# Kernel optimization log

Measured on AMD Instinct MI355X. Metric: run time of the kernel, lower is better.

Reference implementation:

```python
import jax, jax.numpy as jnp
import numpy as np

N_DISEASES = 8192
N_MIRNAS = 16384
N_TOTAL = N_DISEASES + N_MIRNAS
D = 256
B = 65536
K = 50
EPS = 1e-8


def setup_inputs() -> dict:
    key = jax.random.key(0)
    k1, k2, k3, k4, k5, k6 = jax.random.split(key, 6)
    h = jax.random.normal(k1, (N_TOTAL, D), dtype=jnp.float32)
    emb = jax.random.normal(k2, (N_TOTAL, D), dtype=jnp.float32)
    src_init = jax.random.normal(k3, (B, D), dtype=jnp.float32)
    dst_init = jax.random.normal(k4, (B, D), dtype=jnp.float32)
    diseases = jax.random.randint(k5, (B,), 0, N_DISEASES, dtype=jnp.int32)
    mirnas = jax.random.randint(k6, (B,), N_DISEASES, N_TOTAL, dtype=jnp.int32)
    return {"h": h, "emb": emb, "src_init": src_init, "dst_init": dst_init,
            "diseases": diseases, "mirnas": mirnas}


def _cos(a, b):
    # cosine similarity along the last axis, eps-clamped like torch's F.cosine_similarity
    na = jnp.maximum(jnp.linalg.norm(a, axis=-1), EPS)
    nb = jnp.maximum(jnp.linalg.norm(b, axis=-1), EPS)
    return jnp.sum(a * b, axis=-1) / (na * nb)


def _pair_contrastive(pos_sim, neg_sim):
    # -log(exp(pos) / (exp(pos) + exp(neg))) = logaddexp(0, neg - pos)
    return jnp.mean(jnp.logaddexp(jnp.float32(0.0), neg_sim - pos_sim))


def _knn_feature_update(features, k):
    # [N, N] dense similarity, top-(k+1), drop self, gather + mean
    sim = features @ features.T                      # [N, N]
    _, idx = jax.lax.top_k(sim, k + 1)               # [N, k+1]
    idx = idx[:, 1:]                                 # drop self-match
    nbr = features[idx]                              # [N, k, D]
    return jnp.mean(nbr, axis=1)                     # [N, D]


def _knn_contrastive(feat_a, feat_b):
    center_a = jnp.mean(feat_a, axis=0)
    center_b = jnp.mean(feat_b, axis=0)
    sa_a = _cos(feat_a, center_a[None, :])
    sb_a = _cos(feat_a, center_b[None, :])
    loss_a = _pair_contrastive(sa_a, sb_a)
    sb_b = _cos(feat_b, center_b[None, :])
    sa_b = _cos(feat_b, center_a[None, :])
    loss_b = _pair_contrastive(sb_b, sa_b)
    return (loss_a + loss_b) * jnp.float32(0.5)


def reference(h, emb, src_init, dst_init, diseases, mirnas):
    h_d = h[diseases]                                # [B, D]
    h_m = h[mirnas]                                  # [B, D]
    pos_sim = _cos(h_d, src_init)
    neg_sim = _cos(h_d, dst_init)
    contrastive_loss = _pair_contrastive(pos_sim, neg_sim)

    upd_d = _knn_feature_update(emb[:N_DISEASES], K)
    upd_m = _knn_feature_update(emb[N_DISEASES:], K)
    feature_contrastive_loss = _knn_contrastive(upd_d, upd_m)

    # interactionPredictor modeled as sigmoid dot-product scorer
    scores = jax.nn.sigmoid(jnp.sum(h_d * h_m, axis=-1))  # [B]
    return scores, contrastive_loss, feature_contrastive_loss
```

## Files before the change

kernel.cpp:

```cpp
#include <hip/hip_runtime.h>
#include <math.h>

#define NDIS 8192
#define NMIR 16384
#define NTOT 24576
#define DIMD 256
#define BPAIR 65536
#define KSEL 50
#define EPSF 1e-8f
#define CBC 32
#define CAP 80
#define PSTR 320
#define ZD 2.066f
#define ZM 2.418f
#define ZFD 0.9035f
#define ZFM 1.331f
#define NKB 768

typedef __attribute__((ext_vector_type(8))) short bf16x8;
typedef __attribute__((ext_vector_type(4))) float f32x4;
typedef unsigned long long ull;

__device__ __forceinline__ float wredsum(float v) {
#pragma unroll
  for (int off = 1; off < 64; off <<= 1) v += __shfl_xor(v, off, 64);
  return v;
}

__device__ __forceinline__ int wredsumi(int v) {
#pragma unroll
  for (int off = 1; off < 64; off <<= 1) v += __shfl_xor(v, off, 64);
  return v;
}

__device__ __forceinline__ float softplusf(float x) {
  return fmaxf(x, 0.0f) + log1pf(expf(-fabsf(x)));
}

__device__ __forceinline__ float dot4f(const float4 a, const float4 b) {
  return a.x * b.x + a.y * b.y + a.z * b.z + a.w * b.w;
}

__device__ __forceinline__ unsigned short f2bf(float f) {
  unsigned u = __float_as_uint(f);
  unsigned r = (u + 0x7fffu + ((u >> 16) & 1u)) >> 16;
  return (unsigned short)r;
}

__device__ __forceinline__ float b2f(unsigned short x) {
  return __uint_as_float((unsigned)x << 16);
}

__device__ __forceinline__ unsigned ordu(float f) {
  unsigned u = __float_as_uint(f);
  return (u & 0x80000000u) ? ~u : (u | 0x80000000u);
}

__global__ __launch_bounds__(256) void convert_colsum_kernel(
    const float* __restrict__ in, unsigned short* __restrict__ out,
    float* __restrict__ colpart) {
  const int d = threadIdx.x;
  const int r0 = blockIdx.x * 256;
  float s = 0.0f;
  for (int i = 0; i < 256; ++i) {
    const float v = in[(size_t)(r0 + i) * DIMD + d];
    const unsigned short b = f2bf(v);
    out[(size_t)(r0 + i) * DIMD + d] = b;
    s += b2f(b);
  }
  colpart[blockIdx.x * DIMD + d] = s;
}

__global__ __launch_bounds__(256) void tau_kernel(
    const unsigned short* __restrict__ embb, const float* __restrict__ colpart,
    float* __restrict__ tau, float2* __restrict__ musig,
    unsigned* __restrict__ cnts, unsigned* __restrict__ flags) {
  __shared__ float cm[DIMD];
  const int lane = threadIdx.x & 63;
  const int widx = threadIdx.x >> 6;
  const bool bism = blockIdx.x >= 32;
  {
    const int b0 = bism ? 32 : 0, b1 = bism ? 96 : 32;
    const float Ninv = 1.0f / (bism ? (float)NMIR : (float)NDIS);
    float s = 0.0f;
    for (int b = b0; b < b1; ++b) s += colpart[b * DIMD + threadIdx.x];
    cm[threadIdx.x] = s * Ninv;
  }
  __syncthreads();
  const int r0 = blockIdx.x * 256 + widx * 64;
  const float z = bism ? ZM : ZD;
  for (int rr = 0; rr < 64; ++rr) {
    const int row = r0 + rr;
    const float4 cmv = ((const float4*)cm)[lane];
    const ushort4 u = ((const ushort4*)(embb + (size_t)row * DIMD))[lane];
    const float fx = b2f(u.x), fy = b2f(u.y), fz = b2f(u.z), fw = b2f(u.w);
    float dot = fx * cmv.x + fy * cmv.y + fz * cmv.z + fw * cmv.w;
    float nsq = fx * fx + fy * fy + fz * fz + fw * fw;
    dot = wredsum(dot);
    nsq = wredsum(nsq);
    const float sig = sqrtf(nsq);
    if (lane == 0) {
      tau[row] = dot + z * sig;
      musig[row] = make_float2(dot, sig);
      flags[row] = 0u;
    }
    if (lane < 4) cnts[row * 4 + lane] = 0u;
  }
}

__global__ __launch_bounds__(256, 3) void knn_kernel(
    const unsigned short* __restrict__ embb, const float* __restrict__ tau,
    unsigned* __restrict__ part, unsigned* __restrict__ cnts,
    unsigned* __restrict__ flags, const float* __restrict__ h,
    const float* __restrict__ srci, const float* __restrict__ dsti,
    const int* __restrict__ dis, const int* __restrict__ mir,
    float* __restrict__ scores, float* __restrict__ pairpart) {
  __shared__ char lds[3][CBC * 512];
  __shared__ float wsum[4];

  const int tid = threadIdx.x;
  const int lane = tid & 63;
  const int widx = tid >> 6;
  const int q4 = lane >> 4;
  const int l15 = lane & 15;
  const int sh16 = q4 * 16;
  const unsigned lmask = (1u << l15) - 1u;

  const int bid = blockIdx.x;
  const bool ism = bid < 512;
  const int rt = ism ? (bid >> 2) : ((bid - 512) >> 2);
  const int strip = ism ? (bid & 3) : ((bid - 512) & 3);
  const int sw = ism ? 4096 : 2048;
  const int nch = sw / CBC;
  const int gbase = ism ? NDIS : 0;
  const unsigned short* fb = embb + (size_t)gbase * DIMD;

  const int rowbase = rt * 128 + widx * 32;
  const int colstart = strip * sw;
  const char* gb = (const char*)fb;

  bf16x8 afr[2][8];
#pragma unroll
  for (int rg = 0; rg < 2; ++rg) {
    const int arow = rowbase + rg * 16 + l15;
    const char* ab = (const char*)fb + (size_t)arow * 512 + q4 * 16;
#pragma unroll
    for (int kk = 0; kk < 8; ++kk)
      afr[rg][kk] = *(const bf16x8*)(ab + (size_t)kk * 64);
  }

  float tau8[2][4];
  unsigned offb[2];
  int cnt8[2][4];
#pragma unroll
  for (int rg = 0; rg < 2; ++rg) {
    const int db = rowbase + rg * 16 + q4 * 4;
    offb[rg] = (unsigned)(gbase + db) * PSTR + strip * CAP;
#pragma unroll
    for (int j = 0; j < 4; ++j) {
      tau8[rg][j] = tau[gbase + db + j];
      cnt8[rg][j] = 0;
    }
  }

  auto stage = [&](char* dst, int cb0n) {
#pragma unroll
    for (int it = 0; it < 4; ++it) {
      const int m = widx * 4 + it;
      const int col = m * 2 + (lane >> 5);
      const int qq = (lane & 31) * 16;
      const int koff = qq ^ ((col & 7) << 4);
      const char* src = gb + (size_t)(colstart + cb0n + col) * 512 + koff;
      __builtin_amdgcn_global_load_lds(
          (const __attribute__((address_space(1))) void*)src,
          (__attribute__((address_space(3))) void*)(dst + m * 1024), 16, 0, 0);
    }
  };

  char* b0 = lds[0];
  char* b1 = lds[1];
  char* b2 = lds[2];
  stage(b0, 0);
  stage(b1, CBC);
  for (int ch = 0; ch < nch; ++ch) {
    if (ch < nch - 1)
      asm volatile("s_waitcnt vmcnt(4)" ::: "memory");
    else
      asm volatile("s_waitcnt vmcnt(0)" ::: "memory");
    __builtin_amdgcn_sched_barrier(0);
    __builtin_amdgcn_s_barrier();
    __builtin_amdgcn_sched_barrier(0);
    if (ch + 2 < nch) stage(b2, (ch + 2) * CBC);

    const char* bch = b0;
    const int cb0 = ch * CBC;
    f32x4 acc[2][2];
#pragma unroll
    for (int rg = 0; rg < 2; ++rg)
#pragma unroll
      for (int t = 0; t < 2; ++t) acc[rg][t] = (f32x4){0.f, 0.f, 0.f, 0.f};

    __builtin_amdgcn_s_setprio(1);
#pragma unroll
    for (int t = 0; t < 2; ++t) {
      const int col = t * 16 + l15;
      const char* bbase = bch + (size_t)col * 512;
      const int xr = (col & 7) << 4;
#pragma unroll
      for (int kk = 0; kk < 8; ++kk) {
        const int koff = (kk * 64 + (q4 * 16)) ^ xr;
        const bf16x8 b = *(const bf16x8*)(bbase + koff);
        acc[0][t] = __builtin_amdgcn_mfma_f32_16x16x32_bf16(afr[0][kk], b,
                                                            acc[0][t], 0, 0, 0);
        acc[1][t] = __builtin_amdgcn_mfma_f32_16x16x32_bf16(afr[1][kk], b,
                                                            acc[1][t], 0, 0, 0);
      }
    }
    __builtin_amdgcn_s_setprio(0);

#pragma unroll
    for (int t = 0; t < 2; ++t) {
      const int colb = colstart + cb0 + t * 16;
      const unsigned kc = (unsigned)(16383 - (colb + l15));
#pragma unroll
      for (int rg = 0; rg < 2; ++rg) {
        const bool dchr = (colb == rowbase + rg * 16);
#pragma unroll
        for (int j = 0; j < 4; ++j) {
          const float v = acc[rg][t][j];
          bool ok = v > tau8[rg][j];
          if (dchr) ok = ok && (l15 != (q4 * 4 + j));
          const ull m = __ballot(ok);
          if (m) {
            const unsigned m16 = (unsigned)(m >> sh16) & 0xFFFFu;
            const int rank = __popc(m16 & lmask);
            const int slot = cnt8[rg][j] + rank;
            if (ok && slot < CAP)
              part[offb[rg] + (unsigned)(j * PSTR) + slot] =
                  ((ordu(v) >> 14) << 14) | kc;
            cnt8[rg][j] += __popc(m16);
          }
        }
      }
    }

    char* tp = b0; b0 = b1; b1 = b2; b2 = tp;
  }

#pragma unroll
  for (int rg = 0; rg < 2; ++rg) {
#pragma unroll
    for (int j = 0; j < 4; ++j) {
      if (l15 == 0) {
        const int growg = gbase + rowbase + rg * 16 + q4 * 4 + j;
        const int c = cnt8[rg][j];
        cnts[growg * 4 + strip] = (unsigned)(c < CAP ? c : CAP);
        if (c > CAP) flags[growg] = 1u;
      }
    }
  }

  const int gw = bid * 4 + widx;
  float lsum = 0.0f;
  for (int b = gw; b < BPAIR; b += NKB * 4) {
    const int d = dis[b];
    const int m = mir[b];
    const float4 a4 = ((const float4*)(h + (size_t)d * DIMD))[lane];
    const float4 m4 = ((const float4*)(h + (size_t)m * DIMD))[lane];
    const float4 s4 = ((const float4*)(srci + (size_t)b * DIMD))[lane];
    const float4 t4 = ((const float4*)(dsti + (size_t)b * DIMD))[lane];
    float aa = dot4f(a4, a4);
    float ss = dot4f(s4, s4);
    float tt = dot4f(t4, t4);
    float as = dot4f(a4, s4);
    float at = dot4f(a4, t4);
    float am = dot4f(a4, m4);
    aa = wredsum(aa); ss = wredsum(ss); tt = wredsum(tt);
    as = wredsum(as); at = wredsum(at); am = wredsum(am);
    const float ra = fmaxf(sqrtf(aa), EPSF);
    const float pos = as / (ra * fmaxf(sqrtf(ss), EPSF));
    const float neg = at / (ra * fmaxf(sqrtf(tt), EPSF));
    lsum += softplusf(neg - pos);
    if (lane == 0) scores[b] = 1.0f / (1.0f + expf(-am));
  }
  if (lane == 0) wsum[widx] = lsum;
  __syncthreads();
  if (tid == 0)
    pairpart[bid] = (wsum[0] + wsum[1]) + (wsum[2] + wsum[3]);
}

__global__ __launch_bounds__(256) void fallback_kernel(
    const unsigned short* __restrict__ embb, const float2* __restrict__ musig,
    unsigned* __restrict__ part, unsigned* __restrict__ cnts,
    const unsigned* __restrict__ flags, unsigned* __restrict__ fbbuf) {
  __shared__ unsigned short frow[4][DIMD];
  const int lane = threadIdx.x & 63;
  const int widx = threadIdx.x >> 6;
  const int wid = blockIdx.x * 4 + widx;
  const ull bel = (1ull << lane) - 1ull;

  for (int row = wid * 96; row < wid * 96 + 96; ++row) {
    unsigned tot = 0;
    for (int s = 0; s < 4; ++s) tot += cnts[row * 4 + s];
    if (!(flags[row] || tot < KSEL)) continue;

    const bool ism = row >= NDIS;
    const int lrow = ism ? row - NDIS : row;
    const int Ng = ism ? NMIR : NDIS;
    const unsigned short* fb = embb + (ism ? (size_t)NDIS * DIMD : 0);
    const float2 ms = musig[row];
    const float tp = ms.x + (ism ? ZFM : ZFD) * ms.y;

    ((ushort4*)frow[widx])[lane] =
        ((const ushort4*)(fb + (size_t)lrow * DIMD))[lane];

    unsigned* fk = fbbuf + (size_t)wid * 4096;
    int fc = 0;
    for (int cb = 0; cb < Ng; cb += 64) {
      const int col = cb + lane;
      float s = 0.0f;
      for (int d0 = 0; d0 < DIMD; d0 += 4) {
        const ushort4 uc = *(const ushort4*)(fb + (size_t)col * DIMD + d0);
        const ushort4 ur = *(const ushort4*)(&frow[widx][d0]);
        s += b2f(uc.x) * b2f(ur.x) + b2f(uc.y) * b2f(ur.y) +
             b2f(uc.z) * b2f(ur.z) + b2f(uc.w) * b2f(ur.w);
      }
      const bool a = (s > tp) && (col != lrow);
      const ull m = __ballot(a);
      const int sl = fc + __popcll(m & bel);
      if (a && sl < 4096) fk[sl] = ((ordu(s) >> 14) << 14) | (16383u - col);
      fc += __popcll(m);
    }
    if (fc > 4096) fc = 4096;

    unsigned lo = 0u, hi = 0xFFFFFFFFu;
    for (int it = 0; it < 32; ++it) {
      const unsigned mid = lo + ((hi - lo) >> 1);
      int c = 0;
      for (int i = lane; i < fc; i += 64) c += (fk[i] > mid) ? 1 : 0;
      c = wredsumi(c);
      if (c >= KSEL) lo = mid; else hi = mid;
    }
    int wc = 0;
    for (int base = 0; base < fc; base += 64) {
      const int i = base + lane;
      const bool w = (i < fc) && (fk[i] > lo);
      const ull m = __ballot(w);
      const int pos = wc + __popcll(m & bel);
      if (w) part[(size_t)row * PSTR + pos] = fk[i];
      wc += __popcll(m);
    }
    if (lane < 4) cnts[row * 4 + lane] = (lane == 0) ? KSEL : 0u;
  }
}

__global__ __launch_bounds__(256) void merge_kernel(
    const unsigned short* __restrict__ embb, const unsigned* __restrict__ part,
    const unsigned* __restrict__ cnts, float* __restrict__ upd_d,
    float* __restrict__ upd_m) {
  __shared__ unsigned kb[4][PSTR];
  const int lane = threadIdx.x & 63;
  const int widx = threadIdx.x >> 6;
  const int row = blockIdx.x * 4 + widx;
  const bool ism = row >= NDIS;
  const int lrow = ism ? row - NDIS : row;
  const unsigned short* fe = embb + (ism ? (size_t)NDIS * DIMD : 0);
  float* upd =
      (ism ? upd_m + (size_t)lrow * DIMD : upd_d + (size_t)lrow * DIMD);
  const ull bel = (1ull << lane) - 1ull;

  int T = 0;
  for (int s = 0; s < 4; ++s) {
    const int c = (int)cnts[row * 4 + s];
    for (int i = lane; i < c; i += 64)
      kb[widx][T + i] = part[(size_t)row * PSTR + s * CAP + i];
    T += c;
  }
  const int nr = (T + 63) >> 6;
  unsigned k[5];
#pragma unroll
  for (int i = 0; i < 5; ++i) {
    const int idx = i * 64 + lane;
    k[i] = (idx < T) ? kb[widx][idx] : 0u;
  }

  unsigned lo = 0u, hi = 0xFFFFFFFFu;
  for (int it = 0; it < 32; ++it) {
    const unsigned mid = lo + ((hi - lo) >> 1);
    int c = 0;
#pragma unroll
    for (int i = 0; i < 5; ++i)
      if (i < nr) c += __popcll(__ballot(k[i] > mid));
    if (c >= KSEL) lo = mid; else hi = mid;
  }
  int wc = 0;
#pragma unroll
  for (int i = 0; i < 5; ++i) {
    if (i < nr) {
      const bool w = k[i] > lo;
      const ull m = __ballot(w);
      const int pos = wc + __popcll(m & bel);
      if (w) kb[widx][pos] = 16383u - (k[i] & 16383u);
      wc += __popcll(m);
    }
  }

  float ax = 0.f, ay = 0.f, az = 0.f, aw = 0.f;
#pragma unroll 10
  for (int t = 0; t < KSEL; ++t) {
    const int col = (int)kb[widx][t];
    const ushort4 u = ((const ushort4*)(fe + (size_t)col * DIMD))[lane];
    ax += b2f(u.x); ay += b2f(u.y); az += b2f(u.z); aw += b2f(u.w);
  }
  const float inv = 1.0f / (float)KSEL;
  float4 o;
  o.x = ax * inv; o.y = ay * inv; o.z = az * inv; o.w = aw * inv;
  ((float4*)upd)[lane] = o;
}

__global__ __launch_bounds__(256) void center_partial(
    const float* __restrict__ upd, float* __restrict__ part) {
  const int c = threadIdx.x;
  const int r0 = blockIdx.x * 128;
  float s = 0.0f;
  for (int i = 0; i < 128; ++i) s += upd[(size_t)(r0 + i) * DIMD + c];
  part[blockIdx.x * DIMD + c] = s;
}

__global__ __launch_bounds__(256) void center_final(
    const float* __restrict__ part, float* __restrict__ center,
    float* __restrict__ cnorm) {
  const int g = blockIdx.x;
  const int c = threadIdx.x;
  const int b0 = g ? 64 : 0, b1 = g ? 192 : 64;
  const float N = g ? (float)NMIR : (float)NDIS;
  float s = 0.0f;
  for (int b = b0; b < b1; ++b) s += part[b * DIMD + c];
  s /= N;
  center[g * DIMD + c] = s;
  __shared__ float red[256];
  red[c] = s * s;
  __syncthreads();
  for (int off = 128; off > 0; off >>= 1) {
    if (c < off) red[c] += red[c + off];
    __syncthreads();
  }
  if (c == 0) cnorm[g] = sqrtf(red[0]);
}

__global__ __launch_bounds__(256) void knn_loss(
    const float* __restrict__ upd_d, const float* __restrict__ upd_m,
    const float* __restrict__ centers, const float* __restrict__ cnorms,
    float* __restrict__ lpa, float* __restrict__ lpb) {
  const int lane = threadIdx.x & 63;
  const int widx = threadIdx.x >> 6;
  const int bid = blockIdx.x;
  const bool ism = bid >= 128;
  const int lb = ism ? bid - 128 : bid;
  const int N = ism ? NMIR : NDIS;
  const int nw = ism ? 1024 : 512;
  const float* upd = ism ? upd_m : upd_d;
  const int gw = lb * 4 + widx;
  const float4 ca = ((const float4*)centers)[lane];
  const float4 cbv = ((const float4*)(centers + DIMD))[lane];
  const float na = fmaxf(cnorms[0], EPSF);
  const float nb = fmaxf(cnorms[1], EPSF);
  float lsum = 0.0f;
  for (int r = gw; r < N; r += nw) {
    const float4 u = ((const float4*)(upd + (size_t)r * DIMD))[lane];
    float uu = dot4f(u, u);
    float uca = dot4f(u, ca);
    float ucb = dot4f(u, cbv);
    uu = wredsum(uu); uca = wredsum(uca); ucb = wredsum(ucb);
    const float nu = fmaxf(sqrtf(uu), EPSF);
    const float sa = uca / (nu * na);
    const float sb = ucb / (nu * nb);
    const float x = ism ? (sa - sb) : (sb - sa);
    lsum += softplusf(x);
  }
  __shared__ float wsum[4];
  if (lane == 0) wsum[widx] = lsum;
  __syncthreads();
  if (threadIdx.x == 0) {
    const float v = (wsum[0] + wsum[1]) + (wsum[2] + wsum[3]);
    if (ism) lpb[lb] = v; else lpa[lb] = v;
  }
}

__global__ __launch_bounds__(256) void finalize_kernel(
    const float* __restrict__ pairpart, const float* __restrict__ lpa,
    const float* __restrict__ lpb, float* __restrict__ out) {
  __shared__ float red[256];
  const int t = threadIdx.x;

  float s = 0.0f;
  for (int i = t; i < NKB; i += 256) s += pairpart[i];
  red[t] = s;
  __syncthreads();
  for (int off = 128; off > 0; off >>= 1) {
    if (t < off) red[t] += red[t + off];
    __syncthreads();
  }
  const float pairsum = red[0];
  __syncthreads();

  red[t] = (t < 128) ? lpa[t] : 0.0f;
  __syncthreads();
  for (int off = 128; off > 0; off >>= 1) {
    if (t < off) red[t] += red[t + off];
    __syncthreads();
  }
  const float la = red[0];
  __syncthreads();

  red[t] = lpb[t];
  __syncthreads();
  for (int off = 128; off > 0; off >>= 1) {
    if (t < off) red[t] += red[t + off];
    __syncthreads();
  }
  const float lb = red[0];

  if (t == 0) {
    out[BPAIR] = pairsum / (float)BPAIR;
    out[BPAIR + 1] = 0.5f * (la / (float)NDIS + lb / (float)NMIR);
  }
}

extern "C" void kernel_launch(void* const* d_in, const int* in_sizes, int n_in,
                              void* d_out, int out_size, void* d_ws,
                              size_t ws_size, hipStream_t stream) {
  const float* h = (const float*)d_in[0];
  const float* emb = (const float*)d_in[1];
  const float* srci = (const float*)d_in[2];
  const float* dsti = (const float*)d_in[3];
  const int* dis = (const int*)d_in[4];
  const int* mir = (const int*)d_in[5];
  float* out = (float*)d_out;

  float* W = (float*)d_ws;
  float* upd_d = W;
  float* upd_m = upd_d + (size_t)NDIS * DIMD;
  float* pairpart = upd_m + (size_t)NMIR * DIMD;
  float* cpart = pairpart + 1024;
  float* centers = cpart + 192 * DIMD;
  float* cnorms = centers + 512;
  float* lpa = cnorms + 64;
  float* lpb = lpa + 128;
  float* colpart = lpb + 256;
  float* tau = colpart + 96 * DIMD;
  float2* musig = (float2*)(tau + NTOT);
  unsigned* flags = (unsigned*)(musig + NTOT);
  unsigned* cnts = flags + NTOT;
  unsigned short* embb = (unsigned short*)(cnts + NTOT * 4);
  unsigned* part = (unsigned*)(embb + (size_t)NTOT * DIMD);
  unsigned* fbbuf = part + (size_t)NTOT * PSTR;

  convert_colsum_kernel<<<96, 256, 0, stream>>>(emb, embb, colpart);
  tau_kernel<<<96, 256, 0, stream>>>(embb, colpart, tau, musig, cnts, flags);
  knn_kernel<<<NKB, 256, 0, stream>>>(embb, tau, part, cnts, flags, h, srci,
                                      dsti, dis, mir, out, pairpart);
  fallback_kernel<<<64, 256, 0, stream>>>(embb, musig, part, cnts, flags,
                                          fbbuf);
  merge_kernel<<<NTOT / 4, 256, 0, stream>>>(embb, part, cnts, upd_d, upd_m);
  center_partial<<<192, 256, 0, stream>>>(upd_d, cpart);
  center_final<<<2, 256, 0, stream>>>(cpart, centers, cnorms);
  knn_loss<<<384, 256, 0, stream>>>(upd_d, upd_m, centers, cnorms, lpa, lpb);
  finalize_kernel<<<1, 256, 0, stream>>>(pairpart, lpa, lpb, out);
}
```

Baseline: 513.7 us.

## Widen convert grid, add colmean kernel, precompute LDS read offsets in knn

The bf16 convert/column-sum kernel now runs 768 blocks of 32 rows instead of 96 blocks of 256 rows. A new two-block colmean kernel reduces the partial sums once, so tau_kernel no longer re-reduces them in every block. In the knn MFMA loop, the swizzled LDS read addresses are precomputed per lane as even/odd base offsets outside the chunk loop, buffers are addressed by integer offset, and the s_setprio bracketing is removed. The costs are one extra kernel launch and a larger colpart workspace; dropping setprio may change how waves interleave.

```diff
diff --git a/kernel.cpp b/kernel.cpp
--- a/kernel.cpp
+++ b/kernel.cpp
@@ -60,9 +60,9 @@
     const float* __restrict__ in, unsigned short* __restrict__ out,
     float* __restrict__ colpart) {
   const int d = threadIdx.x;
-  const int r0 = blockIdx.x * 256;
+  const int r0 = blockIdx.x * 32;
   float s = 0.0f;
-  for (int i = 0; i < 256; ++i) {
+  for (int i = 0; i < 32; ++i) {
     const float v = in[(size_t)(r0 + i) * DIMD + d];
     const unsigned short b = f2bf(v);
     out[(size_t)(r0 + i) * DIMD + d] = b;
@@ -71,21 +71,26 @@
   colpart[blockIdx.x * DIMD + d] = s;
 }
 
+__global__ __launch_bounds__(256) void colmean_kernel(
+    const float* __restrict__ colpart, float* __restrict__ colmean) {
+  const int g = blockIdx.x;
+  const int d = threadIdx.x;
+  const int b0 = g ? 256 : 0, b1 = g ? 768 : 256;
+  const float Ninv = 1.0f / (g ? (float)NMIR : (float)NDIS);
+  float s = 0.0f;
+  for (int b = b0; b < b1; ++b) s += colpart[b * DIMD + d];
+  colmean[g * DIMD + d] = s * Ninv;
+}
+
 __global__ __launch_bounds__(256) void tau_kernel(
-    const unsigned short* __restrict__ embb, const float* __restrict__ colpart,
+    const unsigned short* __restrict__ embb, const float* __restrict__ colmean,
     float* __restrict__ tau, float2* __restrict__ musig,
     unsigned* __restrict__ cnts, unsigned* __restrict__ flags) {
   __shared__ float cm[DIMD];
   const int lane = threadIdx.x & 63;
   const int widx = threadIdx.x >> 6;
   const bool bism = blockIdx.x >= 32;
-  {
-    const int b0 = bism ? 32 : 0, b1 = bism ? 96 : 32;
-    const float Ninv = 1.0f / (bism ? (float)NMIR : (float)NDIS);
-    float s = 0.0f;
-    for (int b = b0; b < b1; ++b) s += colpart[b * DIMD + threadIdx.x];
-    cm[threadIdx.x] = s * Ninv;
-  }
+  cm[threadIdx.x] = colmean[(bism ? DIMD : 0) + threadIdx.x];
   __syncthreads();
   const int r0 = blockIdx.x * 256 + widx * 64;
   const float z = bism ? ZM : ZD;
@@ -115,7 +120,7 @@
     const float* __restrict__ srci, const float* __restrict__ dsti,
     const int* __restrict__ dis, const int* __restrict__ mir,
     float* __restrict__ scores, float* __restrict__ pairpart) {
-  __shared__ char lds[3][CBC * 512];
+  __shared__ char lds[3 * CBC * 512];
   __shared__ float wsum[4];
 
   const int tid = threadIdx.x;
@@ -149,6 +154,16 @@
       afr[rg][kk] = *(const bf16x8*)(ab + (size_t)kk * 64);
   }
 
+  const int s6 = ((l15 >> 2) & 1) * 64;
+  const int Lc = (q4 * 16) ^ ((l15 & 3) << 4);
+  int vE[2], vO[2];
+#pragma unroll
+  for (int t = 0; t < 2; ++t) {
+    const int base = t * 8192 + l15 * 512 + Lc;
+    vE[t] = base + s6;
+    vO[t] = base - s6;
+  }
+
   float tau8[2][4];
   unsigned offb[2];
   int cnt8[2][4];
@@ -163,7 +178,7 @@
     }
   }
 
-  auto stage = [&](char* dst, int cb0n) {
+  auto stage = [&](int dstOff, int cb0n) {
 #pragma unroll
     for (int it = 0; it < 4; ++it) {
       const int m = widx * 4 + it;
@@ -173,15 +188,14 @@
       const char* src = gb + (size_t)(colstart + cb0n + col) * 512 + koff;
       __builtin_amdgcn_global_load_lds(
           (const __attribute__((address_space(1))) void*)src,
-          (__attribute__((address_space(3))) void*)(dst + m * 1024), 16, 0, 0);
+          (__attribute__((address_space(3))) void*)(lds + dstOff + m * 1024),
+          16, 0, 0);
     }
   };
 
-  char* b0 = lds[0];
-  char* b1 = lds[1];
-  char* b2 = lds[2];
-  stage(b0, 0);
-  stage(b1, CBC);
+  int o0 = 0, o1 = 16384, o2 = 32768;
+  stage(o0, 0);
+  stage(o1, CBC);
   for (int ch = 0; ch < nch; ++ch) {
     if (ch < nch - 1)
       asm volatile("s_waitcnt vmcnt(4)" ::: "memory");
@@ -190,9 +204,8 @@
     __builtin_amdgcn_sched_barrier(0);
     __builtin_amdgcn_s_barrier();
     __builtin_amdgcn_sched_barrier(0);
-    if (ch + 2 < nch) stage(b2, (ch + 2) * CBC);
-
-    const char* bch = b0;
+    if (ch + 2 < nch) stage(o2, (ch + 2) * CBC);
+
     const int cb0 = ch * CBC;
     f32x4 acc[2][2];
 #pragma unroll
@@ -200,23 +213,24 @@
 #pragma unroll
       for (int t = 0; t < 2; ++t) acc[rg][t] = (f32x4){0.f, 0.f, 0.f, 0.f};
 
-    __builtin_amdgcn_s_setprio(1);
 #pragma unroll
     for (int t = 0; t < 2; ++t) {
-      const int col = t * 16 + l15;
-      const char* bbase = bch + (size_t)col * 512;
-      const int xr = (col & 7) << 4;
-#pragma unroll
-      for (int kk = 0; kk < 8; ++kk) {
-        const int koff = (kk * 64 + (q4 * 16)) ^ xr;
-        const bf16x8 b = *(const bf16x8*)(bbase + koff);
-        acc[0][t] = __builtin_amdgcn_mfma_f32_16x16x32_bf16(afr[0][kk], b,
+      const char* pE = lds + o0 + vE[t];
+      const char* pO = lds + o0 + vO[t];
+#pragma unroll
+      for (int kp = 0; kp < 4; ++kp) {
+        const bf16x8 be = *(const bf16x8*)(pE + kp * 128);
+        acc[0][t] = __builtin_amdgcn_mfma_f32_16x16x32_bf16(afr[0][2 * kp], be,
                                                             acc[0][t], 0, 0, 0);
-        acc[1][t] = __builtin_amdgcn_mfma_f32_16x16x32_bf16(afr[1][kk], b,
+        acc[1][t] = __builtin_amdgcn_mfma_f32_16x16x32_bf16(afr[1][2 * kp], be,
                                                             acc[1][t], 0, 0, 0);
+        const bf16x8 bo = *(const bf16x8*)(pO + 64 + kp * 128);
+        acc[0][t] = __builtin_amdgcn_mfma_f32_16x16x32_bf16(
+            afr[0][2 * kp + 1], bo, acc[0][t], 0, 0, 0);
+        acc[1][t] = __builtin_amdgcn_mfma_f32_16x16x32_bf16(
+            afr[1][2 * kp + 1], bo, acc[1][t], 0, 0, 0);
       }
     }
-    __builtin_amdgcn_s_setprio(0);
 
 #pragma unroll
     for (int t = 0; t < 2; ++t) {
@@ -244,7 +258,7 @@
       }
     }
 
-    char* tp = b0; b0 = b1; b1 = b2; b2 = tp;
+    const int tp = o0; o0 = o1; o1 = o2; o2 = tp;
   }
 
 #pragma unroll
@@ -548,7 +562,8 @@
   float* lpa = cnorms + 64;
   float* lpb = lpa + 128;
   float* colpart = lpb + 256;
-  float* tau = colpart + 96 * DIMD;
+  float* colmean = colpart + 768 * DIMD;
+  float* tau = colmean + 512;
   float2* musig = (float2*)(tau + NTOT);
   unsigned* flags = (unsigned*)(musig + NTOT);
   unsigned* cnts = flags + NTOT;
@@ -556,8 +571,9 @@
   unsigned* part = (unsigned*)(embb + (size_t)NTOT * DIMD);
   unsigned* fbbuf = part + (size_t)NTOT * PSTR;
 
-  convert_colsum_kernel<<<96, 256, 0, stream>>>(emb, embb, colpart);
-  tau_kernel<<<96, 256, 0, stream>>>(embb, colpart, tau, musig, cnts, flags);
+  convert_colsum_kernel<<<768, 256, 0, stream>>>(emb, embb, colpart);
+  colmean_kernel<<<2, 256, 0, stream>>>(colpart, colmean);
+  tau_kernel<<<96, 256, 0, stream>>>(embb, colmean, tau, musig, cnts, flags);
   knn_kernel<<<NKB, 256, 0, stream>>>(embb, tau, part, cnts, flags, h, srci,
                                       dsti, dis, mir, out, pairpart);
   fallback_kernel<<<64, 256, 0, stream>>>(embb, musig, part, cnts, flags,
```

Result: slower. 563.2 us (+9.6%).
